# Kernel tuning notes

Measured on AMD Instinct MI355X. Metric: run time of the kernel, lower is better.

Reference implementation:

```python
import jax, jax.numpy as jnp
import numpy as np
import math

B, T, C, H = 2, 2048, 1024, 16
D = C // H  # head dim = 64


def setup_inputs() -> dict:
    key = jax.random.key(0)
    ks = jax.random.split(key, 9)
    s = 1.0 / math.sqrt(C)
    inp = {
        "x": jax.random.normal(ks[0], (B, T, C), dtype=jnp.float32),
        "Wk": jax.random.normal(ks[1], (C, C), dtype=jnp.float32) * s,
        "bk": jax.random.normal(ks[2], (C,), dtype=jnp.float32) * s,
        "Wq": jax.random.normal(ks[3], (C, C), dtype=jnp.float32) * s,
        "bq": jax.random.normal(ks[4], (C,), dtype=jnp.float32) * s,
        "Wv": jax.random.normal(ks[5], (C, C), dtype=jnp.float32) * s,
        "bv": jax.random.normal(ks[6], (C,), dtype=jnp.float32) * s,
        "Wo": jax.random.normal(ks[7], (C, C), dtype=jnp.float32) * s,
        "bo": jax.random.normal(ks[8], (C,), dtype=jnp.float32) * s,
    }
    return inp


def reference(x, Wk, bk, Wq, bq, Wv, bv, Wo, bo):
    # QKV projections, split heads: [B,T,C] -> [B,H,T,D]
    def proj(W, b):
        return (x @ W.T + b).reshape(B, T, H, D).transpose(0, 2, 1, 3)

    k = proj(Wk, bk)
    q = proj(Wq, bq)
    v = proj(Wv, bv)

    # NOTE: original scales by 1/sqrt(embedding_dim), not head_dim
    scale = 1.0 / math.sqrt(C)
    scores = jnp.einsum("bhtd,bhsd->bhts", q, k) * scale  # [B,H,T,T]
    causal = jnp.tril(jnp.ones((T, T), dtype=bool))
    scores = jnp.where(causal[None, None], scores, -jnp.inf)
    attn = jax.nn.softmax(scores, axis=-1)
    y = jnp.einsum("bhts,bhsd->bhtd", attn, v)  # [B,H,T,D]
    y = y.transpose(0, 2, 1, 3).reshape(B, T, C)
    return y @ Wo.T + bo
```

## Files before the change

kernel.cpp:

```cpp
#include <hip/hip_runtime.h>
#include <hip/hip_bf16.h>
#include <stdint.h>
#include <stddef.h>

#define B_ 2
#define T_ 2048
#define C_ 1024
#define H_ 16
#define D_ 64
#define M_ (B_*T_)

typedef __attribute__((ext_vector_type(8))) short short8;
typedef __attribute__((ext_vector_type(4))) float f32x4;
typedef __attribute__((ext_vector_type(16))) float f32x16;
typedef __attribute__((ext_vector_type(4))) unsigned int u32x4;

__device__ __forceinline__ unsigned short f2bf(float f) {
    unsigned u = __float_as_uint(f);
    unsigned r = 0x7FFFu + ((u >> 16) & 1u);
    return (unsigned short)((u + r) >> 16);
}

__device__ __forceinline__ unsigned cvtpk_bf16(float lo, float hi) {
    unsigned r;
    asm("v_cvt_pk_bf16_f32 %0, %1, %2" : "=v"(r) : "v"(lo), "v"(hi));
    return r;
}

__device__ __forceinline__ float fexp2(float x) {
    float r;
    asm("v_exp_f32 %0, %1" : "=v"(r) : "v"(x));
    return r;
}

__device__ __forceinline__ void plswap(unsigned &a, unsigned &b) {
    asm("v_permlane32_swap_b32 %0, %1" : "+v"(a), "+v"(b));
}

__device__ __forceinline__ float xhalf_max(float v) {
    float a = v, b = v;
    asm("" : "+v"(b));
    asm("v_permlane32_swap_b32 %0, %1" : "+v"(a), "+v"(b));
    return fmaxf(a, b);
}
__device__ __forceinline__ float xhalf_sum(float v) {
    float a = v, b = v;
    asm("" : "+v"(b));
    asm("v_permlane32_swap_b32 %0, %1" : "+v"(a), "+v"(b));
    return a + b;
}

__device__ __forceinline__ void gload16(const void* g, void* l) {
    __builtin_amdgcn_global_load_lds(
        (__attribute__((address_space(1))) void*)g,
        (__attribute__((address_space(3))) void*)l,
        16, 0, 0);
}

__global__ void cvt_all(const float* __restrict__ x,  const float* __restrict__ wk,
                        const float* __restrict__ wq, const float* __restrict__ wv,
                        const float* __restrict__ wo,
                        unsigned short* __restrict__ xb,  unsigned short* __restrict__ wkb,
                        unsigned short* __restrict__ wqb, unsigned short* __restrict__ wvb,
                        unsigned short* __restrict__ wob) {
    int idx = (blockIdx.x * blockDim.x + threadIdx.x) * 4;
    const float* in; unsigned short* out; int off;
    if      (idx < (4<<20)) { in = x;  out = xb;  off = idx; }
    else if (idx < (5<<20)) { in = wk; out = wkb; off = idx - (4<<20); }
    else if (idx < (6<<20)) { in = wq; out = wqb; off = idx - (5<<20); }
    else if (idx < (7<<20)) { in = wv; out = wvb; off = idx - (6<<20); }
    else                    { in = wo; out = wob; off = idx - (7<<20); }
    float4 v = *reinterpret_cast<const float4*>(in + off);
    ushort4 o;
    o.x = f2bf(v.x); o.y = f2bf(v.y); o.z = f2bf(v.z); o.w = f2bf(v.w);
    *reinterpret_cast<ushort4*>(out + off) = o;
}

__global__ __launch_bounds__(256) void gemm_qkv(
    const unsigned short* __restrict__ A,
    const unsigned short* __restrict__ W0,
    const unsigned short* __restrict__ W1,
    const unsigned short* __restrict__ W2,
    const float* __restrict__ b0,
    const float* __restrict__ b1,
    const float* __restrict__ b2,
    unsigned short* __restrict__ o0,
    unsigned short* __restrict__ o1,
    unsigned short* __restrict__ o2)
{
    __shared__ unsigned short As[128*32];
    __shared__ unsigned short Bs[128*32];
    int which = blockIdx.x >> 8;
    int bx = blockIdx.x & 255;
    int bm = bx >> 3, bn = bx & 7;
    const unsigned short* W = (which==0) ? W0 : ((which==1) ? W1 : W2);
    const float* bias = (which==0) ? b0 : ((which==1) ? b1 : b2);

    int tid = threadIdx.x;
    int lane = tid & 63;
    int fr = lane & 15, fq = lane >> 4;
    int wid = tid >> 6;
    int wr = wid >> 1, wc = wid & 1;

    int srow = tid >> 2;
    int scol = (tid & 3) << 3;
    const unsigned short* Ab = A + (size_t)(bm*128 + srow) * C_ + scol;
    const unsigned short* Wb = W + (size_t)(bn*128 + srow) * C_ + scol;

    f32x4 acc[4][4] = {};

    for (int kt = 0; kt < C_/32; ++kt) {
        int ko = kt*32;
        gload16(Ab + ko,            &As[tid*8]);
        gload16(Ab + 64*C_ + ko,    &As[2048 + tid*8]);
        gload16(Wb + ko,            &Bs[tid*8]);
        gload16(Wb + 64*C_ + ko,    &Bs[2048 + tid*8]);
        __syncthreads();
        short8 af[4], bfr[4];
        #pragma unroll
        for (int i = 0; i < 4; ++i) {
            af[i]  = *reinterpret_cast<const short8*>(&As[(wr*64 + i*16 + fr)*32 + fq*8]);
            bfr[i] = *reinterpret_cast<const short8*>(&Bs[(wc*64 + i*16 + fr)*32 + fq*8]);
        }
        #pragma unroll
        for (int i = 0; i < 4; ++i)
            #pragma unroll
            for (int j = 0; j < 4; ++j)
                acc[i][j] = __builtin_amdgcn_mfma_f32_16x16x32_bf16(af[i], bfr[j], acc[i][j], 0, 0, 0);
        __syncthreads();
    }

    float sc = (which == 1) ? 0.045084220f : 1.0f;
    int mbase = bm*128 + wr*64;
    int nbase = bn*128 + wc*64;
    #pragma unroll
    for (int j = 0; j < 4; ++j) {
        int col = nbase + j*16 + fr;
        float bv = bias[col];
        int h = col >> 6, d = col & 63;
        #pragma unroll
        for (int i = 0; i < 4; ++i) {
            int r0 = mbase + i*16 + fq*4;
            #pragma unroll
            for (int r = 0; r < 4; ++r) {
                float v = (acc[i][j][r] + bv) * sc;
                int m = r0 + r;
                int b = m >> 11, t = m & (T_-1);
                unsigned short hv = f2bf(v);
                if (which == 2)
                    o2[((size_t)(b*H_ + h)*D_ + d)*T_ + t] = hv;
                else {
                    unsigned short* o = (which==0) ? o0 : o1;
                    o[((size_t)(b*H_ + h)*T_ + t)*D_ + d] = hv;
                }
            }
        }
    }
}

__global__ __launch_bounds__(256, 6) void gemm_out(
    const unsigned short* __restrict__ A,
    const unsigned short* __restrict__ W,
    const float* __restrict__ bias,
    float* __restrict__ out)
{
    __shared__ unsigned short As[64*32];
    __shared__ unsigned short Bs[128*32];
    int bx = blockIdx.x;
    int bm = bx >> 3, bn = bx & 7;

    int tid = threadIdx.x;
    int lane = tid & 63;
    int fr = lane & 15, fq = lane >> 4;
    int wid = tid >> 6;
    int wr = wid >> 1, wc = wid & 1;

    int arow = tid >> 2;
    int acol = (tid & 3) << 3;
    const unsigned short* Ab = A + (size_t)(bm*64 + arow) * C_ + acol;
    const unsigned short* Wb = W + (size_t)(bn*128 + arow) * C_ + acol;

    f32x4 acc[2][4] = {};

    for (int kt = 0; kt < C_/32; ++kt) {
        int ko = kt*32;
        gload16(Ab + ko,            &As[tid*8]);
        gload16(Wb + ko,            &Bs[tid*8]);
        gload16(Wb + 64*C_ + ko,    &Bs[2048 + tid*8]);
        __syncthreads();
        short8 af[2], bfr[4];
        #pragma unroll
        for (int i = 0; i < 2; ++i)
            af[i]  = *reinterpret_cast<const short8*>(&As[(wr*32 + i*16 + fr)*32 + fq*8]);
        #pragma unroll
        for (int j = 0; j < 4; ++j)
            bfr[j] = *reinterpret_cast<const short8*>(&Bs[(wc*64 + j*16 + fr)*32 + fq*8]);
        #pragma unroll
        for (int i = 0; i < 2; ++i)
            #pragma unroll
            for (int j = 0; j < 4; ++j)
                acc[i][j] = __builtin_amdgcn_mfma_f32_16x16x32_bf16(af[i], bfr[j], acc[i][j], 0, 0, 0);
        __syncthreads();
    }

    int mbase = bm*64 + wr*32;
    int nbase = bn*128 + wc*64;
    #pragma unroll
    for (int j = 0; j < 4; ++j) {
        int col = nbase + j*16 + fr;
        float bv = bias[col];
        #pragma unroll
        for (int i = 0; i < 2; ++i) {
            int r0 = mbase + i*16 + fq*4;
            #pragma unroll
            for (int r = 0; r < 4; ++r)
                out[(size_t)(r0 + r)*C_ + col] = acc[i][j][r] + bv;
        }
    }
}

__device__ __forceinline__ void attn_subtile(
    const short8 (&kf)[4], const short8 (&qf)[4],
    const short8 (&vlo)[2], const short8 (&vhi)[2],
    bool diag, int l31, int hi,
    f32x16& o0, f32x16& o1, float& m_, float& l_)
{
    f32x16 a0 = {};
    __builtin_amdgcn_s_setprio(1);
    a0 = __builtin_amdgcn_mfma_f32_32x32x16_bf16(kf[0], qf[0], a0, 0, 0, 0);
    a0 = __builtin_amdgcn_mfma_f32_32x32x16_bf16(kf[1], qf[1], a0, 0, 0, 0);
    a0 = __builtin_amdgcn_mfma_f32_32x32x16_bf16(kf[2], qf[2], a0, 0, 0, 0);
    a0 = __builtin_amdgcn_mfma_f32_32x32x16_bf16(kf[3], qf[3], a0, 0, 0, 0);
    __builtin_amdgcn_s_setprio(0);

    if (diag) {
        #pragma unroll
        for (int r = 0; r < 16; ++r) {
            int kvl = (r&3) + 8*(r>>2) + 4*hi;
            if (kvl > l31) a0[r] = -1e30f;
        }
    }

    float x0 = fmaxf(a0[0], a0[1]),   x1 = fmaxf(a0[2], a0[3]);
    float x2 = fmaxf(a0[4], a0[5]),   x3 = fmaxf(a0[6], a0[7]);
    float x4 = fmaxf(a0[8], a0[9]),   x5 = fmaxf(a0[10], a0[11]);
    float x6 = fmaxf(a0[12], a0[13]), x7 = fmaxf(a0[14], a0[15]);
    float y0 = fmaxf(x0, x1), y1 = fmaxf(x2, x3), y2 = fmaxf(x4, x5), y3 = fmaxf(x6, x7);
    float pm = fmaxf(fmaxf(y0, y1), fmaxf(y2, y3));
    pm = xhalf_max(pm);

    if (!__all(pm - m_ <= 8.0f)) {
        float mn = fmaxf(m_, pm);
        float alpha = fexp2(m_ - mn);
        l_ *= alpha;
        m_ = mn;
        #pragma unroll
        for (int r = 0; r < 16; ++r) {
            int row = (r&3) + 8*(r>>2) + 4*hi;
            float ar = __shfl(alpha, row);
            o0[r] *= ar;
            o1[r] *= ar;
        }
    }

    #pragma unroll
    for (int r = 0; r < 16; ++r)
        a0[r] = fexp2(a0[r] - m_);
    float s0 = a0[0]+a0[1],  s1 = a0[2]+a0[3],  s2 = a0[4]+a0[5],   s3 = a0[6]+a0[7];
    float s4 = a0[8]+a0[9],  s5 = a0[10]+a0[11], s6 = a0[12]+a0[13], s7 = a0[14]+a0[15];
    float u0 = s0+s1, u1 = s2+s3, u2 = s4+s5, u3 = s6+s7;
    float rs = (u0+u1) + (u2+u3);
    rs = xhalf_sum(rs);
    l_ += rs;

    unsigned pk_[8];
    #pragma unroll
    for (int jj = 0; jj < 8; ++jj)
        pk_[jj] = cvtpk_bf16(a0[2*jj], a0[2*jj+1]);

    #pragma unroll
    for (int kb = 0; kb < 2; ++kb) {
        unsigned fx = pk_[4*kb+0], fz = pk_[4*kb+2];
        unsigned fy = pk_[4*kb+1], fw = pk_[4*kb+3];
        plswap(fx, fz);
        plswap(fy, fw);
        u32x4 wv;
        wv.x = fx; wv.y = fy; wv.z = fz; wv.w = fw;
        short8 pfrag = __builtin_bit_cast(short8, wv);
        __builtin_amdgcn_s_setprio(1);
        o0 = __builtin_amdgcn_mfma_f32_32x32x16_bf16(pfrag, vlo[kb], o0, 0, 0, 0);
        o1 = __builtin_amdgcn_mfma_f32_32x32x16_bf16(pfrag, vhi[kb], o1, 0, 0, 0);
        __builtin_amdgcn_s_setprio(0);
    }
}

__global__ __launch_bounds__(256, 2) void flash_attn(
    const unsigned short* __restrict__ q,
    const unsigned short* __restrict__ k,
    const unsigned short* __restrict__ vt,
    unsigned short* __restrict__ y)
{
    __shared__ __align__(16) unsigned short ST[2][4][4096];
    float* oP  = reinterpret_cast<float*>(&ST[0][0][0]);
    float* mlP = oP + 4*32*68;

    int tid = threadIdx.x, lane = tid & 63, w = tid >> 6;
    int l31 = lane & 31, hi = lane >> 5, rsw = l31 & 7;
    int role = w >> 1, pair = w & 1;
    int bid = blockIdx.x;

    int half = bid >> 8;
    int idx  = bid & 255;
    int bh   = (idx & 7)*4 + ((idx >> 3) & 3);
    int sidx = idx >> 5;
    int S    = half ? sidx : (15 - sidx);

    const unsigned short* kp = k  + (size_t)bh*T_*D_;
    const unsigned short* vp = vt + (size_t)bh*D_*T_;

    int rowbase = S*128 + pair*64;
    const unsigned short* qp = q + ((size_t)bh*T_ + rowbase) * D_;

    short8 qf0[4], qf1[4];
    #pragma unroll
    for (int dk = 0; dk < 4; ++dk) {
        qf0[dk] = *reinterpret_cast<const short8*>(qp + (size_t)l31*D_        + dk*16 + hi*8);
        qf1[dk] = *reinterpret_cast<const short8*>(qp + (size_t)(32 + l31)*D_ + dk*16 + hi*8);
    }

    f32x16 o00 = {}, o01 = {}, o10 = {}, o11 = {};
    float m0 = -1e30f, l0 = 0.f, m1 = -1e30f, l1 = 0.f;

    int lim0 = 4*S + 2*pair;
    int lim1 = lim0 + 1;
    int niter = S + 1;

    #define STAGE(ii, bufi)                                                            \
    {                                                                                  \
        _Pragma("unroll")                                                              \
        for (int jj = 0; jj < 2; ++jj) {                                               \
            int c2 = tid + jj*256;                                                     \
            int row_ = c2 >> 3;                                                        \
            int slot_ = (c2 & 7) ^ (row_ & 7);                                         \
            int tl_ = (ii), th_ = S + 1 + (ii);                                        \
            gload16(kp + ((size_t)(tl_*64 + row_))*D_ + slot_*8, &ST[bufi][0][c2*8]);  \
            gload16(kp + ((size_t)(th_*64 + row_))*D_ + slot_*8, &ST[bufi][1][c2*8]);  \
            gload16(vp + (size_t)row_*T_ + tl_*64 + slot_*8,     &ST[bufi][2][c2*8]);  \
            gload16(vp + (size_t)row_*T_ + th_*64 + slot_*8,     &ST[bufi][3][c2*8]);  \
        }                                                                              \
    }

    STAGE(0, 0);
    __syncthreads();

    for (int i = 0; i < niter; ++i) {
        int bufi = i & 1;
        if (i + 1 < niter) STAGE(i + 1, bufi ^ 1);

        const unsigned short* Kl = &ST[bufi][role][0];
        const unsigned short* Vl = &ST[bufi][2 + role][0];
        int t = role ? (S + 1 + i) : i;

        #pragma unroll
        for (int st = 0; st < 2; ++st) {
            int g = 2*t + st;
            if (g <= lim1) {
                short8 kf[4];
                const unsigned short* kr = Kl + (st*32 + l31)*64;
                #pragma unroll
                for (int dk = 0; dk < 4; ++dk)
                    kf[dk] = *reinterpret_cast<const short8*>(kr + (((dk<<1)|hi) ^ rsw)*8);
                short8 vlo[2], vhi[2];
                const unsigned short* vr0 = Vl + l31*64;
                const unsigned short* vr1 = Vl + (32 + l31)*64;
                #pragma unroll
                for (int kb = 0; kb < 2; ++kb) {
                    int sl = (((st<<2) | (kb<<1) | hi) ^ rsw) * 8;
                    vlo[kb] = *reinterpret_cast<const short8*>(vr0 + sl);
                    vhi[kb] = *reinterpret_cast<const short8*>(vr1 + sl);
                }
                if (g <= lim0)
                    attn_subtile(kf, qf0, vlo, vhi, g == lim0, l31, hi, o00, o01, m0, l0);
                attn_subtile(kf, qf1, vlo, vhi, g == lim1, l31, hi, o10, o11, m1, l1);
            }
        }
        __syncthreads();
    }
    #undef STAGE

    if (!role) {
        int s0 = pair*2, s1 = pair*2 + 1;
        #pragma unroll
        for (int rr = 0; rr < 16; ++rr) {
            int crow = (rr&3) + 8*(rr>>2) + 4*hi;
            oP[(s0*32 + crow)*68 + l31]      = o00[rr];
            oP[(s0*32 + crow)*68 + 32 + l31] = o01[rr];
            oP[(s1*32 + crow)*68 + l31]      = o10[rr];
            oP[(s1*32 + crow)*68 + 32 + l31] = o11[rr];
        }
        if (!hi) {
            mlP[s0*32 + l31]       = m0;
            mlP[128 + s0*32 + l31] = l0;
            mlP[s1*32 + l31]       = m1;
            mlP[128 + s1*32 + l31] = l1;
        }
    }
    __syncthreads();
    if (role) {
        int b = bh >> 4, h = bh & 15;
        #pragma unroll
        for (int qq = 0; qq < 2; ++qq) {
            int set = pair*2 + qq;
            const f32x16& po0 = qq ? o10 : o00;
            const f32x16& po1 = qq ? o11 : o01;
            float m_ = qq ? m1 : m0;
            float l_ = qq ? l1 : l0;

            float mA = mlP[set*32 + l31];
            float lA = mlP[128 + set*32 + l31];
            float mN = fmaxf(mA, m_);
            float aA = fexp2(mA - mN);
            float aB = fexp2(m_ - mN);
            float lN = lA*aA + l_*aB;
            float inv = 1.0f / lN;
            float cA = aA * inv, cB = aB * inv;

            #pragma unroll
            for (int rr = 0; rr < 16; ++rr) {
                int crow = (rr&3) + 8*(rr>>2) + 4*hi;
                float cAr = __shfl(cA, crow);
                float cBr = __shfl(cB, crow);
                float vA0 = oP[(set*32 + crow)*68 + l31];
                float vA1 = oP[(set*32 + crow)*68 + 32 + l31];
                int trow = rowbase + qq*32 + crow;
                size_t base = ((size_t)(b*T_ + trow))*C_ + h*64;
                y[base + l31]      = f2bf(vA0*cAr + po0[rr]*cBr);
                y[base + 32 + l31] = f2bf(vA1*cAr + po1[rr]*cBr);
            }
        }
    }
}

extern "C" void kernel_launch(void* const* d_in, const int* in_sizes, int n_in,
                              void* d_out, int out_size, void* d_ws, size_t ws_size,
                              hipStream_t stream) {
    const float* x  = (const float*)d_in[0];
    const float* Wk = (const float*)d_in[1];
    const float* bk = (const float*)d_in[2];
    const float* Wq = (const float*)d_in[3];
    const float* bq = (const float*)d_in[4];
    const float* Wv = (const float*)d_in[5];
    const float* bv = (const float*)d_in[6];
    const float* Wo = (const float*)d_in[7];
    const float* bo = (const float*)d_in[8];
    float* out = (float*)d_out;

    char* ws = (char*)d_ws;
    unsigned short* xb  = (unsigned short*)(ws);
    unsigned short* wkb = (unsigned short*)(ws + ((size_t)8  << 20));
    unsigned short* wqb = (unsigned short*)(ws + ((size_t)10 << 20));
    unsigned short* wvb = (unsigned short*)(ws + ((size_t)12 << 20));
    unsigned short* wob = (unsigned short*)(ws + ((size_t)14 << 20));
    unsigned short* qb  = (unsigned short*)(ws + ((size_t)16 << 20));
    unsigned short* kb  = (unsigned short*)(ws + ((size_t)24 << 20));
    unsigned short* vtb = (unsigned short*)(ws + ((size_t)32 << 20));
    unsigned short* yb  = (unsigned short*)(ws + ((size_t)40 << 20));

    cvt_all<<<dim3(8192), dim3(256), 0, stream>>>(
        x, Wk, Wq, Wv, Wo, xb, wkb, wqb, wvb, wob);

    gemm_qkv<<<dim3(768), dim3(256), 0, stream>>>(xb, wkb, wqb, wvb, bk, bq, bv, kb, qb, vtb);

    flash_attn<<<dim3(512), dim3(256), 0, stream>>>(qb, kb, vtb, yb);

    gemm_out<<<dim3(512), dim3(256), 0, stream>>>(yb, wob, bo, out);
}
```

Measured before the change: 107.1 us.

## Halve flash-attention query tile to 64 rows and double grid for occupancy

Each attention block now owns 64 query rows instead of 128, with each wave handling one 32-row query strip and one of two split-K halves, using 32-key tiles and a smaller LDS footprint. The grid doubles to 1024 blocks and launch bounds allow four blocks per CU, aiming for better occupancy and load balance across the causal triangle. The final merge of the two split halves is rewritten so all threads cooperate and emit vectorized 16-byte bf16 stores. Smaller tiles mean more synchronization per key processed and less reuse of each staged K/V tile.

```diff
diff --git a/kernel.cpp b/kernel.cpp
--- a/kernel.cpp
+++ b/kernel.cpp
@@ -294,60 +294,60 @@
     }
 }
 
-__global__ __launch_bounds__(256, 2) void flash_attn(
+__global__ __launch_bounds__(256, 4) void flash_attn(
     const unsigned short* __restrict__ q,
     const unsigned short* __restrict__ k,
     const unsigned short* __restrict__ vt,
     unsigned short* __restrict__ y)
 {
-    __shared__ __align__(16) unsigned short ST[2][4][4096];
-    float* oP  = reinterpret_cast<float*>(&ST[0][0][0]);
-    float* mlP = oP + 4*32*68;
+    __shared__ __align__(16) char LDSRAW[35840];
+    unsigned short (*ST)[4][2048] = reinterpret_cast<unsigned short(*)[4][2048]>(LDSRAW);
+    float* oP = reinterpret_cast<float*>(LDSRAW);
+    float* mP = oP + 4*32*68;
+    float* lP = mP + 128;
 
     int tid = threadIdx.x, lane = tid & 63, w = tid >> 6;
     int l31 = lane & 31, hi = lane >> 5, rsw = l31 & 7;
-    int role = w >> 1, pair = w & 1;
+    int p = w & 1, s = w >> 1;
     int bid = blockIdx.x;
 
-    int half = bid >> 8;
-    int idx  = bid & 255;
+    int half = bid >> 9;
+    int idx  = bid & 511;
     int bh   = (idx & 7)*4 + ((idx >> 3) & 3);
-    int sidx = idx >> 5;
-    int S    = half ? sidx : (15 - sidx);
+    int jidx = idx >> 5;
+    int j    = half ? jidx : (31 - jidx);
 
     const unsigned short* kp = k  + (size_t)bh*T_*D_;
     const unsigned short* vp = vt + (size_t)bh*D_*T_;
-
-    int rowbase = S*128 + pair*64;
+    int b = bh >> 4, h = bh & 15;
+
+    int rowbase = j*64 + p*32;
     const unsigned short* qp = q + ((size_t)bh*T_ + rowbase) * D_;
 
-    short8 qf0[4], qf1[4];
-    #pragma unroll
-    for (int dk = 0; dk < 4; ++dk) {
-        qf0[dk] = *reinterpret_cast<const short8*>(qp + (size_t)l31*D_        + dk*16 + hi*8);
-        qf1[dk] = *reinterpret_cast<const short8*>(qp + (size_t)(32 + l31)*D_ + dk*16 + hi*8);
-    }
-
-    f32x16 o00 = {}, o01 = {}, o10 = {}, o11 = {};
-    float m0 = -1e30f, l0 = 0.f, m1 = -1e30f, l1 = 0.f;
-
-    int lim0 = 4*S + 2*pair;
-    int lim1 = lim0 + 1;
-    int niter = S + 1;
-
-    #define STAGE(ii, bufi)                                                            \
-    {                                                                                  \
-        _Pragma("unroll")                                                              \
-        for (int jj = 0; jj < 2; ++jj) {                                               \
-            int c2 = tid + jj*256;                                                     \
-            int row_ = c2 >> 3;                                                        \
-            int slot_ = (c2 & 7) ^ (row_ & 7);                                         \
-            int tl_ = (ii), th_ = S + 1 + (ii);                                        \
-            gload16(kp + ((size_t)(tl_*64 + row_))*D_ + slot_*8, &ST[bufi][0][c2*8]);  \
-            gload16(kp + ((size_t)(th_*64 + row_))*D_ + slot_*8, &ST[bufi][1][c2*8]);  \
-            gload16(vp + (size_t)row_*T_ + tl_*64 + slot_*8,     &ST[bufi][2][c2*8]);  \
-            gload16(vp + (size_t)row_*T_ + th_*64 + slot_*8,     &ST[bufi][3][c2*8]);  \
-        }                                                                              \
+    short8 qf[4];
+    #pragma unroll
+    for (int dk = 0; dk < 4; ++dk)
+        qf[dk] = *reinterpret_cast<const short8*>(qp + (size_t)l31*D_ + dk*16 + hi*8);
+
+    f32x16 o0 = {}, o1 = {};
+    float m_ = -1e30f, l_ = 0.f;
+
+    int lim = 2*j + p;
+    int niter = j + 1;
+    int gbase = s ? (j + 1) : 0;
+
+    #define STAGE(ii, bufi)                                                           \
+    {                                                                                 \
+        int c2 = tid;                                                                 \
+        int krow = c2 >> 3;                                                           \
+        int kslot = (c2 & 7) ^ (krow & 7);                                            \
+        int vrow = c2 >> 2;                                                           \
+        int vslot = (c2 & 3) ^ (vrow & 3);                                            \
+        int tl_ = (ii), th_ = j + 1 + (ii);                                           \
+        gload16(kp + ((size_t)(tl_*32 + krow))*D_ + kslot*8, &ST[bufi][0][c2*8]);     \
+        gload16(kp + ((size_t)(th_*32 + krow))*D_ + kslot*8, &ST[bufi][1][c2*8]);     \
+        gload16(vp + (size_t)vrow*T_ + tl_*32 + vslot*8,     &ST[bufi][2][c2*8]);     \
+        gload16(vp + (size_t)vrow*T_ + th_*32 + vslot*8,     &ST[bufi][3][c2*8]);     \
     }
 
     STAGE(0, 0);
@@ -357,86 +357,64 @@
         int bufi = i & 1;
         if (i + 1 < niter) STAGE(i + 1, bufi ^ 1);
 
-        const unsigned short* Kl = &ST[bufi][role][0];
-        const unsigned short* Vl = &ST[bufi][2 + role][0];
-        int t = role ? (S + 1 + i) : i;
-
-        #pragma unroll
-        for (int st = 0; st < 2; ++st) {
-            int g = 2*t + st;
-            if (g <= lim1) {
-                short8 kf[4];
-                const unsigned short* kr = Kl + (st*32 + l31)*64;
-                #pragma unroll
-                for (int dk = 0; dk < 4; ++dk)
-                    kf[dk] = *reinterpret_cast<const short8*>(kr + (((dk<<1)|hi) ^ rsw)*8);
-                short8 vlo[2], vhi[2];
-                const unsigned short* vr0 = Vl + l31*64;
-                const unsigned short* vr1 = Vl + (32 + l31)*64;
-                #pragma unroll
-                for (int kb = 0; kb < 2; ++kb) {
-                    int sl = (((st<<2) | (kb<<1) | hi) ^ rsw) * 8;
-                    vlo[kb] = *reinterpret_cast<const short8*>(vr0 + sl);
-                    vhi[kb] = *reinterpret_cast<const short8*>(vr1 + sl);
-                }
-                if (g <= lim0)
-                    attn_subtile(kf, qf0, vlo, vhi, g == lim0, l31, hi, o00, o01, m0, l0);
-                attn_subtile(kf, qf1, vlo, vhi, g == lim1, l31, hi, o10, o11, m1, l1);
+        int g = gbase + i;
+        if (g <= lim) {
+            const unsigned short* Kl = &ST[bufi][s][0];
+            const unsigned short* Vl = &ST[bufi][2 + s][0];
+            short8 kf[4];
+            #pragma unroll
+            for (int dk = 0; dk < 4; ++dk)
+                kf[dk] = *reinterpret_cast<const short8*>(
+                    Kl + l31*64 + ((((dk<<1)|hi)) ^ rsw)*8);
+            short8 vlo[2], vhi[2];
+            #pragma unroll
+            for (int kb = 0; kb < 2; ++kb) {
+                int sl = ((((kb<<1)|hi)) ^ (l31 & 3)) * 8;
+                vlo[kb] = *reinterpret_cast<const short8*>(Vl + l31*32 + sl);
+                vhi[kb] = *reinterpret_cast<const short8*>(Vl + (32 + l31)*32 + sl);
             }
+            attn_subtile(kf, qf, vlo, vhi, g == lim, l31, hi, o0, o1, m_, l_);
         }
         __syncthreads();
     }
     #undef STAGE
 
-    if (!role) {
-        int s0 = pair*2, s1 = pair*2 + 1;
+    {
+        int set = (s << 1) | p;
         #pragma unroll
         for (int rr = 0; rr < 16; ++rr) {
             int crow = (rr&3) + 8*(rr>>2) + 4*hi;
-            oP[(s0*32 + crow)*68 + l31]      = o00[rr];
-            oP[(s0*32 + crow)*68 + 32 + l31] = o01[rr];
-            oP[(s1*32 + crow)*68 + l31]      = o10[rr];
-            oP[(s1*32 + crow)*68 + 32 + l31] = o11[rr];
-        }
-        if (!hi) {
-            mlP[s0*32 + l31]       = m0;
-            mlP[128 + s0*32 + l31] = l0;
-            mlP[s1*32 + l31]       = m1;
-            mlP[128 + s1*32 + l31] = l1;
-        }
+            oP[(set*32 + crow)*68 + l31]      = o0[rr];
+            oP[(set*32 + crow)*68 + 32 + l31] = o1[rr];
+        }
+        if (!hi) { mP[set*32 + l31] = m_; lP[set*32 + l31] = l_; }
     }
     __syncthreads();
-    if (role) {
-        int b = bh >> 4, h = bh & 15;
-        #pragma unroll
-        for (int qq = 0; qq < 2; ++qq) {
-            int set = pair*2 + qq;
-            const f32x16& po0 = qq ? o10 : o00;
-            const f32x16& po1 = qq ? o11 : o01;
-            float m_ = qq ? m1 : m0;
-            float l_ = qq ? l1 : l0;
-
-            float mA = mlP[set*32 + l31];
-            float lA = mlP[128 + set*32 + l31];
-            float mN = fmaxf(mA, m_);
+    {
+        int qr = tid >> 3;
+        int dc = tid & 7;
+        #pragma unroll
+        for (int ch = 0; ch < 2; ++ch) {
+            int sA = ch, sB = 2 + ch;
+            float mA = mP[sA*32 + qr], mB = mP[sB*32 + qr];
+            float lA = lP[sA*32 + qr], lB = lP[sB*32 + qr];
+            float mN = fmaxf(mA, mB);
             float aA = fexp2(mA - mN);
-            float aB = fexp2(m_ - mN);
-            float lN = lA*aA + l_*aB;
+            float aB = fexp2(mB - mN);
+            float lN = lA*aA + lB*aB;
             float inv = 1.0f / lN;
             float cA = aA * inv, cB = aB * inv;
 
-            #pragma unroll
-            for (int rr = 0; rr < 16; ++rr) {
-                int crow = (rr&3) + 8*(rr>>2) + 4*hi;
-                float cAr = __shfl(cA, crow);
-                float cBr = __shfl(cB, crow);
-                float vA0 = oP[(set*32 + crow)*68 + l31];
-                float vA1 = oP[(set*32 + crow)*68 + 32 + l31];
-                int trow = rowbase + qq*32 + crow;
-                size_t base = ((size_t)(b*T_ + trow))*C_ + h*64;
-                y[base + l31]      = f2bf(vA0*cAr + po0[rr]*cBr);
-                y[base + 32 + l31] = f2bf(vA1*cAr + po1[rr]*cBr);
+            unsigned short yv[8];
+            #pragma unroll
+            for (int e = 0; e < 8; ++e) {
+                float acc = cA * oP[(sA*32 + qr)*68 + dc*8 + e]
+                          + cB * oP[(sB*32 + qr)*68 + dc*8 + e];
+                yv[e] = f2bf(acc);
             }
+            int trow = j*64 + ch*32 + qr;
+            size_t base = ((size_t)(b*T_ + trow))*C_ + h*64 + dc*8;
+            *reinterpret_cast<short8*>(y + base) = *reinterpret_cast<short8*>(yv);
         }
     }
 }
@@ -471,7 +449,7 @@
 
     gemm_qkv<<<dim3(768), dim3(256), 0, stream>>>(xb, wkb, wqb, wvb, bk, bq, bv, kb, qb, vtb);
 
-    flash_attn<<<dim3(512), dim3(256), 0, stream>>>(qb, kb, vtb, yb);
+    flash_attn<<<dim3(1024), dim3(256), 0, stream>>>(qb, kb, vtb, yb);
 
     gemm_out<<<dim3(512), dim3(256), 0, stream>>>(yb, wob, bo, out);
 }
```

Result: faster. 102.9 us, median of 2 (-4.0%).
